# Optimization experiments

Measured on AMD Instinct MI355X. Metric: run time of the kernel, lower is better.

The kernel has to match this reference:

```python
import jax, jax.numpy as jnp
import numpy as np


def _attn_chunk(q, k, v, scale):
    # q: [b,s,h,d], k/v: [b,c,h,d] (one ring chunk)
    scores = jnp.einsum('bqhd,bkhd->bhqk', q, k) * scale
    lse = jax.nn.logsumexp(scores, axis=-1)            # [b,h,q]
    p = jnp.exp(scores - lse[..., None])               # [b,h,q,k]
    out = jnp.einsum('bhqk,bkhd->bqhd', p, v)          # [b,q,h,d]
    lse = jnp.transpose(lse, (0, 2, 1))[..., None]     # [b,q,h,1] for broadcast
    return out, lse


def setup_inputs() -> dict:
    key = jax.random.key(0)
    kq, kk, kv = jax.random.split(key, 3)
    B, S, H, D = 1, 4096, 16, 128
    q = jax.random.normal(kq, (B, S, H, D), dtype=jnp.float32)
    k = jax.random.normal(kk, (B, S, H, D), dtype=jnp.float32)
    v = jax.random.normal(kv, (B, S, H, D), dtype=jnp.float32)
    return {'q': q, 'k': k, 'v': v, 'ring_size': 4}


def reference(q, k, v, ring_size):
    # Ring attention forward: iterate over ring_size KV chunks, merging
    # partial (out, lse) with the sigmoid/logsigmoid online-softmax update
    # from update_out_and_lse_pass_q.
    B, S, H, D = q.shape
    R = int(ring_size)
    C = S // R
    scale = 1.0 / jnp.sqrt(jnp.asarray(D, dtype=q.dtype))
    k_chunks = k.reshape(B, R, C, H, D)
    v_chunks = v.reshape(B, R, C, H, D)

    # first ring step initializes the accumulators
    out, lse = _attn_chunk(q, k_chunks[:, 0], v_chunks[:, 0], scale)
    out = out.astype(jnp.float32)
    for r in range(1, R):
        block_out, block_lse = _attn_chunk(q, k_chunks[:, r], v_chunks[:, r], scale)
        block_out = block_out.astype(jnp.float32)
        # update_out_and_lse_pass_q
        out = out - jax.nn.sigmoid(block_lse - lse) * (out - block_out)
        lse = lse - jax.nn.log_sigmoid(lse - block_lse)
    return out
```

## Files before the change

kernel.cpp:

```cpp
#include <hip/hip_runtime.h>


#define S_LEN 4096
#define NH    16
#define DH    128
#define QT    128
#define KT    32
#define KSTR  136
#define VTS   40
#define QSTR  136
#define PSTR  40

typedef short bf16x8 __attribute__((ext_vector_type(8)));
typedef float floatx16 __attribute__((ext_vector_type(16)));

__device__ __forceinline__ unsigned short f2bf(float f) {
  union { float f; unsigned u; } x; x.f = f;
  unsigned r = x.u + 0x7FFFu + ((x.u >> 16) & 1u);
  return (unsigned short)(r >> 16);
}

__device__ __forceinline__ void gll16(const unsigned short* g, unsigned short* l) {
  __builtin_amdgcn_global_load_lds(
      (const __attribute__((address_space(1))) void*)g,
      (__attribute__((address_space(3))) void*)l, 16, 0, 0);
}

__global__ __launch_bounds__(256) void conv_k(const float* __restrict__ Kg,
                                              unsigned short* __restrict__ Kb) {
  int idx = blockIdx.x * 256 + threadIdx.x;
  int d4 = idx & 31;
  int h  = (idx >> 5) & 15;
  int s  = idx >> 9;
  float4 a = ((const float4*)Kg)[idx];
  ushort4 o = make_ushort4(f2bf(a.x), f2bf(a.y), f2bf(a.z), f2bf(a.w));
  ((ushort4*)Kb)[(((size_t)h * S_LEN + s) << 5) + d4] = o;
}

__global__ __launch_bounds__(256) void conv_v(const float* __restrict__ Vg,
                                              unsigned short* __restrict__ Vt) {
  __shared__ unsigned short sT[DH * VTS];
  const int c = blockIdx.x;
  const int h = blockIdx.y;
  const int t = threadIdx.x;
  {
    const int key = t >> 3;
    const int d0  = (t & 7) * 16;
    const int g   = (key >> 2) & 3;
    const int pos = (key & 3) | ((((g & 1) << 1) | (g >> 1)) << 2) | (key & 16);
    const float* src = Vg + (((size_t)(c * KT + key) * NH + h) * DH + d0);
#pragma unroll
    for (int i = 0; i < 4; ++i) {
      float4 a = ((const float4*)src)[i];
      sT[(d0 + 4 * i + 0) * VTS + pos] = f2bf(a.x);
      sT[(d0 + 4 * i + 1) * VTS + pos] = f2bf(a.y);
      sT[(d0 + 4 * i + 2) * VTS + pos] = f2bf(a.z);
      sT[(d0 + 4 * i + 3) * VTS + pos] = f2bf(a.w);
    }
  }
  __syncthreads();
  {
    const int d = t >> 1, hf = t & 1;
    uint4 w0 = *(const uint4*)&sT[d * VTS + hf * 16];
    uint4 w1 = *(const uint4*)&sT[d * VTS + hf * 16 + 8];
    size_t ob = ((size_t)(h * DH + d)) * S_LEN + c * KT + hf * 16;
    *(uint4*)&Vt[ob]     = w0;
    *(uint4*)&Vt[ob + 8] = w1;
  }
}

__global__ __launch_bounds__(256, 2) void fa_fwd3(
    const float* __restrict__ Qg, const unsigned short* __restrict__ Kb,
    const unsigned short* __restrict__ Vt, float* __restrict__ Og) {
  __shared__ __align__(16) unsigned short sK[2][4096];
  __shared__ __align__(16) unsigned short sV[2][4096];

  const int tid  = threadIdx.x;
  const int lane = tid & 63;
  const int wave = tid >> 6;
  const int f  = blockIdx.x;
  const int i  = f >> 3;
  const int h  = (f & 7) + 8 * (i & 1);
  const int q0 = (i >> 1) * QT;

  const unsigned short* Kh = Kb + (size_t)h * S_LEN * DH;
  const unsigned short* Vh = Vt + (size_t)h * DH * S_LEN;

  int skoff[2], svoff[2];
#pragma unroll
  for (int s = 0; s < 2; ++s) {
    const int ii = wave * 2 + s;
    { const int C = ii * 64 + lane;
      const int m = C >> 4;
      const int j = (lane & 15) ^ (m & 15);
      skoff[s] = m * DH + j * 8; }
    { const int C = ii * 64 + lane;
      const int r = C >> 2;
      const int j = (lane & 3) ^ ((r >> 1) & 3);
      svoff[s] = r * S_LEN + j * 8; }
  }
  const int ldst = wave * 1024;

  const int m31 = lane & 31, hh = lane >> 5;
  int kro[8], vro[8];
#pragma unroll
  for (int kc = 0; kc < 8; ++kc)
    kro[kc] = m31 * 128 + (((2 * kc + hh) ^ (m31 & 15)) * 8);
#pragma unroll
  for (int dt = 0; dt < 4; ++dt)
#pragma unroll
    for (int ff = 0; ff < 2; ++ff) {
      const int r = dt * 32 + m31;
      vro[dt * 2 + ff] = r * 32 + (((2 * ff + hh) ^ ((r >> 1) & 3)) * 8);
    }

  bf16x8 qf[8];
  {
    const float* qr = Qg +
        ((size_t)(q0 + wave * 32 + m31) * NH + h) * DH + hh * 8;
#pragma unroll
    for (int kc = 0; kc < 8; ++kc) {
      float4 a = *(const float4*)(qr + kc * 16);
      float4 b = *(const float4*)(qr + kc * 16 + 4);
      bf16x8 q;
      q[0] = f2bf(a.x); q[1] = f2bf(a.y); q[2] = f2bf(a.z); q[3] = f2bf(a.w);
      q[4] = f2bf(b.x); q[5] = f2bf(b.y); q[6] = f2bf(b.z); q[7] = f2bf(b.w);
      qf[kc] = q;
    }
  }

  floatx16 oacc[4];
#pragma unroll
  for (int dt = 0; dt < 4; ++dt)
#pragma unroll
    for (int j = 0; j < 16; ++j) oacc[dt][j] = 0.f;
  float ssum = 0.f;

#define ISSUE(BK, BV, KTV)                                                    \
  {                                                                           \
    _Pragma("unroll") for (int s = 0; s < 2; ++s) {                           \
      gll16(Kh + (size_t)(KTV) * DH + skoff[s], &(BK)[ldst + s * 512]);       \
      gll16(Vh + (KTV) + svoff[s], &(BV)[ldst + s * 512]);                    \
    }                                                                         \
  }

#define COMPUTE_TILE(KB, VB)                                                  \
  {                                                                           \
    floatx16 sc;                                                              \
    _Pragma("unroll") for (int j = 0; j < 16; ++j) sc[j] = 0.f;               \
    _Pragma("unroll") for (int kc = 0; kc < 8; ++kc) {                        \
      bf16x8 kf = *(const bf16x8*)((KB) + kro[kc]);                           \
      sc = __builtin_amdgcn_mfma_f32_32x32x16_bf16(kf, qf[kc], sc, 0, 0, 0);  \
    }                                                                         \
    float p[16];                                                              \
    _Pragma("unroll") for (int j = 0; j < 16; ++j) {                          \
      p[j] = __expf(fmaf(sc[j], 0.08838834764831845f, 0.0019512177f));        \
      ssum += p[j];                                                           \
    }                                                                         \
    bf16x8 pf0, pf1;                                                          \
    unsigned* u0 = (unsigned*)&pf0;                                           \
    unsigned* u1 = (unsigned*)&pf1;                                           \
    _Pragma("unroll") for (int m = 0; m < 4; ++m) {                           \
      u0[m] = (__float_as_uint(p[2 * m + 1]) & 0xFFFF0000u) |                 \
              (__float_as_uint(p[2 * m]) >> 16);                              \
      u1[m] = (__float_as_uint(p[2 * m + 9]) & 0xFFFF0000u) |                 \
              (__float_as_uint(p[2 * m + 8]) >> 16);                          \
    }                                                                         \
    _Pragma("unroll") for (int dt = 0; dt < 4; ++dt) {                        \
      bf16x8 v0 = *(const bf16x8*)((VB) + vro[dt * 2]);                       \
      bf16x8 v1 = *(const bf16x8*)((VB) + vro[dt * 2 + 1]);                   \
      oacc[dt] =                                                              \
          __builtin_amdgcn_mfma_f32_32x32x16_bf16(pf0, v0, oacc[dt], 0, 0, 0);\
      oacc[dt] =                                                              \
          __builtin_amdgcn_mfma_f32_32x32x16_bf16(pf1, v1, oacc[dt], 0, 0, 0);\
    }                                                                         \
  }

  ISSUE(sK[0], sV[0], 0);
  __syncthreads();
  for (int t = 0; t < 64; ++t) {
    ISSUE(sK[1], sV[1], 64 * t + 32);
    COMPUTE_TILE(sK[0], sV[0]);
    __syncthreads();
    if (t < 63) ISSUE(sK[0], sV[0], 64 * t + 64);
    COMPUTE_TILE(sK[1], sV[1]);
    __syncthreads();
  }
#undef ISSUE
#undef COMPUTE_TILE

  float tot  = ssum + __shfl_xor(ssum, 32);
  float vinv = 1.0f / tot;
  const int rb = hh * 4;
#pragma unroll
  for (int j = 0; j < 16; ++j) {
    const int row = (j & 3) + 8 * (j >> 2) + rb;
    const float inv = __shfl(vinv, row);
    float* op = Og + ((size_t)(q0 + wave * 32 + row) * NH + h) * DH + m31;
#pragma unroll
    for (int dt = 0; dt < 4; ++dt) op[dt * 32] = oacc[dt][j] * inv;
  }
}

__global__ __launch_bounds__(256, 2) void fa_fwd_v1(
    const float* __restrict__ Qg, const float* __restrict__ Kg,
    const float* __restrict__ Vg, float* __restrict__ Og)
{
  __shared__ unsigned short sQ[QT * QSTR];
  __shared__ unsigned short sK1[KT * KSTR];
  __shared__ unsigned short sVT1[DH * VTS];
  __shared__ unsigned short sP[4][32 * PSTR];
  const int tid  = threadIdx.x;
  const int lane = tid & 63;
  const int wave = tid >> 6;
  const int h    = blockIdx.y;
  const int q0   = blockIdx.x * QT;
  {
    const int row = tid >> 1;
    const int db  = (tid & 1) * 64;
    const float* gq = Qg + ((size_t)(q0 + row) * NH + h) * DH + db;
    unsigned short* dst = &sQ[row * QSTR + db];
#pragma unroll
    for (int i = 0; i < 16; ++i) {
      float4 a = ((const float4*)gq)[i];
      *(ushort4*)(dst + 4 * i) =
          make_ushort4(f2bf(a.x), f2bf(a.y), f2bf(a.z), f2bf(a.w));
    }
  }
  __syncthreads();
  bf16x8 qf[8];
  {
    const unsigned short* qr =
        &sQ[(wave * 32 + (lane & 31)) * QSTR + ((lane >> 5) * 8)];
#pragma unroll
    for (int kc = 0; kc < 8; ++kc) qf[kc] = *(const bf16x8*)(qr + kc * 16);
  }
  floatx16 oacc[4];
  float sl[16];
#pragma unroll
  for (int j = 0; j < 16; ++j) sl[j] = 0.f;
#pragma unroll
  for (int dt = 0; dt < 4; ++dt)
#pragma unroll
    for (int j = 0; j < 16; ++j) oacc[dt][j] = 0.f;
  for (int kt = 0; kt < S_LEN; kt += KT) {
    __syncthreads();
    {
      const int key = tid >> 3;
      const int db  = (tid & 7) * 16;
      const float* gk = Kg + ((size_t)(kt + key) * NH + h) * DH + db;
      unsigned short* dst = &sK1[key * KSTR + db];
#pragma unroll
      for (int i = 0; i < 4; ++i) {
        float4 a = ((const float4*)gk)[i];
        *(ushort4*)(dst + 4 * i) =
            make_ushort4(f2bf(a.x), f2bf(a.y), f2bf(a.z), f2bf(a.w));
      }
    }
    {
      const int kp = tid & 15;
      const int db = (tid >> 4) * 8;
      const float* g0 = Vg + ((size_t)(kt + 2 * kp) * NH + h) * DH + db;
      const float* g1 = g0 + (size_t)NH * DH;
      float4 a0 = ((const float4*)g0)[0], b0 = ((const float4*)g0)[1];
      float4 a1 = ((const float4*)g1)[0], b1 = ((const float4*)g1)[1];
      float e0[8] = {a0.x, a0.y, a0.z, a0.w, b0.x, b0.y, b0.z, b0.w};
      float e1[8] = {a1.x, a1.y, a1.z, a1.w, b1.x, b1.y, b1.z, b1.w};
      unsigned* dw = (unsigned*)sVT1;
#pragma unroll
      for (int j = 0; j < 8; ++j)
        dw[(db + j) * (VTS / 2) + kp] =
            (unsigned)f2bf(e0[j]) | ((unsigned)f2bf(e1[j]) << 16);
    }
    __syncthreads();
    floatx16 sc;
#pragma unroll
    for (int j = 0; j < 16; ++j) sc[j] = 0.f;
    {
      const unsigned short* kb = &sK1[(lane & 31) * KSTR + ((lane >> 5) * 8)];
#pragma unroll
      for (int kc = 0; kc < 8; ++kc) {
        bf16x8 bf = *(const bf16x8*)(kb + kc * 16);
        sc = __builtin_amdgcn_mfma_f32_32x32x16_bf16(qf[kc], bf, sc, 0, 0, 0);
      }
    }
    unsigned short pw[16];
#pragma unroll
    for (int j = 0; j < 16; ++j) {
      float p = __expf(sc[j] * 0.08838834764831845f);
      sl[j] += p;
      pw[j] = f2bf(p);
    }
    {
      unsigned short* pb = sP[wave];
      const int col = lane & 31;
      const int rb  = (lane >> 5) * 4;
#pragma unroll
      for (int j = 0; j < 16; ++j) {
        const int row = (j & 3) + 8 * (j >> 2) + rb;
        pb[row * PSTR + col] = pw[j];
      }
    }
    __syncthreads();
    bf16x8 pf0, pf1;
    {
      const unsigned short* pr =
          &sP[wave][(lane & 31) * PSTR + ((lane >> 5) * 8)];
      pf0 = *(const bf16x8*)(pr);
      pf1 = *(const bf16x8*)(pr + 16);
    }
#pragma unroll
    for (int dt = 0; dt < 4; ++dt) {
      const unsigned short* vb =
          &sVT1[(dt * 32 + (lane & 31)) * VTS + ((lane >> 5) * 8)];
      bf16x8 v0 = *(const bf16x8*)(vb);
      bf16x8 v1 = *(const bf16x8*)(vb + 16);
      oacc[dt] = __builtin_amdgcn_mfma_f32_32x32x16_bf16(pf0, v0, oacc[dt], 0, 0, 0);
      oacc[dt] = __builtin_amdgcn_mfma_f32_32x32x16_bf16(pf1, v1, oacc[dt], 0, 0, 0);
    }
  }
#pragma unroll
  for (int j = 0; j < 16; ++j) {
    float s = sl[j];
    s += __shfl_xor(s, 1);
    s += __shfl_xor(s, 2);
    s += __shfl_xor(s, 4);
    s += __shfl_xor(s, 8);
    s += __shfl_xor(s, 16);
    sl[j] = 1.0f / s;
  }
  {
    const int col = lane & 31;
    const int rb  = (lane >> 5) * 4;
#pragma unroll
    for (int j = 0; j < 16; ++j) {
      const int row = (j & 3) + 8 * (j >> 2) + rb;
      float* op = Og + ((size_t)(q0 + wave * 32 + row) * NH + h) * DH + col;
#pragma unroll
      for (int dt = 0; dt < 4; ++dt)
        op[dt * 32] = oacc[dt][j] * sl[j];
    }
  }
}

extern "C" void kernel_launch(void* const* d_in, const int* in_sizes, int n_in,
                              void* d_out, int out_size, void* d_ws, size_t ws_size,
                              hipStream_t stream) {
  const float* q = (const float*)d_in[0];
  const float* k = (const float*)d_in[1];
  const float* v = (const float*)d_in[2];
  float* o = (float*)d_out;
  const size_t elems = (size_t)NH * S_LEN * DH;
  const size_t need  = 2 * elems * sizeof(unsigned short);
  if (ws_size >= need) {
    unsigned short* Kb = (unsigned short*)d_ws;
    unsigned short* Vt = Kb + elems;
    conv_k<<<(int)(elems / 4 / 256), 256, 0, stream>>>(k, Kb);
    conv_v<<<dim3(S_LEN / KT, NH), 256, 0, stream>>>(v, Vt);
    fa_fwd3<<<512, 256, 0, stream>>>(q, Kb, Vt, o);
  } else {
    fa_fwd_v1<<<dim3(S_LEN / QT, NH), 256, 0, stream>>>(q, k, v, o);
  }
}
```

Baseline: 277.2 us.

## Split waves across key halves, reuse K/V fragments for two query tiles, merge in LDS

The main kernel now has each wave handle 64 query rows (two 32-row MFMA tiles) over half of each 64-key tile. Every K and V fragment read from LDS feeds two MFMAs, and LDS stages double to 64 KB with a shared-memory reduction of partial outputs and row sums at the end. The V transpose kernel drops its LDS staging and writes packed bf16 pairs straight to global memory. The bf16 packing uses a byte-permute instruction. The larger LDS footprint and doubled accumulators raise register and LDS pressure, which may limit occupancy, and the final merge adds extra synchronisation.

```diff
diff --git a/kernel.cpp b/kernel.cpp
--- a/kernel.cpp
+++ b/kernel.cpp
@@ -5,7 +5,6 @@
 #define NH    16
 #define DH    128
 #define QT    128
-#define KT    32
 #define KSTR  136
 #define VTS   40
 #define QSTR  136
@@ -18,6 +17,9 @@
   union { float f; unsigned u; } x; x.f = f;
   unsigned r = x.u + 0x7FFFu + ((x.u >> 16) & 1u);
   return (unsigned short)(r >> 16);
+}
+__device__ __forceinline__ unsigned packbf(float a, float b) {
+  return (unsigned)f2bf(a) | ((unsigned)f2bf(b) << 16);
 }
 
 __device__ __forceinline__ void gll16(const unsigned short* g, unsigned short* l) {
@@ -38,46 +40,39 @@
 }
 
 __global__ __launch_bounds__(256) void conv_v(const float* __restrict__ Vg,
-                                              unsigned short* __restrict__ Vt) {
-  __shared__ unsigned short sT[DH * VTS];
-  const int c = blockIdx.x;
-  const int h = blockIdx.y;
-  const int t = threadIdx.x;
-  {
-    const int key = t >> 3;
-    const int d0  = (t & 7) * 16;
-    const int g   = (key >> 2) & 3;
-    const int pos = (key & 3) | ((((g & 1) << 1) | (g >> 1)) << 2) | (key & 16);
-    const float* src = Vg + (((size_t)(c * KT + key) * NH + h) * DH + d0);
-#pragma unroll
-    for (int i = 0; i < 4; ++i) {
-      float4 a = ((const float4*)src)[i];
-      sT[(d0 + 4 * i + 0) * VTS + pos] = f2bf(a.x);
-      sT[(d0 + 4 * i + 1) * VTS + pos] = f2bf(a.y);
-      sT[(d0 + 4 * i + 2) * VTS + pos] = f2bf(a.z);
-      sT[(d0 + 4 * i + 3) * VTS + pos] = f2bf(a.w);
-    }
-  }
-  __syncthreads();
-  {
-    const int d = t >> 1, hf = t & 1;
-    uint4 w0 = *(const uint4*)&sT[d * VTS + hf * 16];
-    uint4 w1 = *(const uint4*)&sT[d * VTS + hf * 16 + 8];
-    size_t ob = ((size_t)(h * DH + d)) * S_LEN + c * KT + hf * 16;
-    *(uint4*)&Vt[ob]     = w0;
-    *(uint4*)&Vt[ob + 8] = w1;
-  }
-}
-
-__global__ __launch_bounds__(256, 2) void fa_fwd3(
+                                              unsigned* __restrict__ Vtd) {
+  const int c  = blockIdx.x;
+  const int hd = blockIdx.y;
+  const int t  = threadIdx.x;
+  const int kp   = t & 15;
+  const int d0   = (t >> 4) * 8;
+  const int key0 = 2 * kp;
+  const int g    = (key0 >> 2) & 3;
+  const int pos0 = (key0 & 3) | ((((g & 1) << 1) | (g >> 1)) << 2) | (key0 & 16);
+  const float* s0 = Vg + ((size_t)(c * 32 + key0) * NH + hd) * DH + d0;
+  const float* s1 = s0 + (size_t)NH * DH;
+  float4 a0 = ((const float4*)s0)[0], b0 = ((const float4*)s0)[1];
+  float4 a1 = ((const float4*)s1)[0], b1 = ((const float4*)s1)[1];
+  float e0[8] = {a0.x, a0.y, a0.z, a0.w, b0.x, b0.y, b0.z, b0.w};
+  float e1[8] = {a1.x, a1.y, a1.z, a1.w, b1.x, b1.y, b1.z, b1.w};
+  unsigned* dst = Vtd + ((size_t)(hd * DH + d0)) * (S_LEN / 2) + c * 16 + (pos0 >> 1);
+#pragma unroll
+  for (int j = 0; j < 8; ++j)
+    dst[j * (S_LEN / 2)] = packbf(e0[j], e1[j]);
+}
+
+__global__ __launch_bounds__(256, 2) void fa_fwd4(
     const float* __restrict__ Qg, const unsigned short* __restrict__ Kb,
     const unsigned short* __restrict__ Vt, float* __restrict__ Og) {
-  __shared__ __align__(16) unsigned short sK[2][4096];
-  __shared__ __align__(16) unsigned short sV[2][4096];
+  __shared__ __align__(16) unsigned char smem[65536];
+  unsigned short* sKb = (unsigned short*)smem;
+  unsigned short* sVb = (unsigned short*)(smem + 32768);
 
   const int tid  = threadIdx.x;
   const int lane = tid & 63;
   const int wave = tid >> 6;
+  const int qg   = wave >> 1;
+  const int kh   = wave & 1;
   const int f  = blockIdx.x;
   const int i  = f >> 3;
   const int h  = (f & 7) + 8 * (i & 1);
@@ -89,13 +84,11 @@
   int skoff[2], svoff[2];
 #pragma unroll
   for (int s = 0; s < 2; ++s) {
-    const int ii = wave * 2 + s;
-    { const int C = ii * 64 + lane;
-      const int m = C >> 4;
+    const int C = (wave * 2 + s) * 64 + lane;
+    { const int m = C >> 4;
       const int j = (lane & 15) ^ (m & 15);
       skoff[s] = m * DH + j * 8; }
-    { const int C = ii * 64 + lane;
-      const int r = C >> 2;
+    { const int r = C >> 2;
       const int j = (lane & 3) ^ ((r >> 1) & 3);
       svoff[s] = r * S_LEN + j * 8; }
   }
@@ -113,11 +106,14 @@
       const int r = dt * 32 + m31;
       vro[dt * 2 + ff] = r * 32 + (((2 * ff + hh) ^ ((r >> 1) & 3)) * 8);
     }
-
-  bf16x8 qf[8];
-  {
+  const unsigned short* kBase[2] = {sKb + kh * 4096, sKb + 8192 + kh * 4096};
+  const unsigned short* vBase[2] = {sVb + kh * 4096, sVb + 8192 + kh * 4096};
+
+  bf16x8 qf[2][8];
+#pragma unroll
+  for (int s = 0; s < 2; ++s) {
     const float* qr = Qg +
-        ((size_t)(q0 + wave * 32 + m31) * NH + h) * DH + hh * 8;
+        ((size_t)(q0 + qg * 64 + s * 32 + m31) * NH + h) * DH + hh * 8;
 #pragma unroll
     for (int kc = 0; kc < 8; ++kc) {
       float4 a = *(const float4*)(qr + kc * 16);
@@ -125,80 +121,128 @@
       bf16x8 q;
       q[0] = f2bf(a.x); q[1] = f2bf(a.y); q[2] = f2bf(a.z); q[3] = f2bf(a.w);
       q[4] = f2bf(b.x); q[5] = f2bf(b.y); q[6] = f2bf(b.z); q[7] = f2bf(b.w);
-      qf[kc] = q;
-    }
-  }
-
-  floatx16 oacc[4];
-#pragma unroll
-  for (int dt = 0; dt < 4; ++dt)
-#pragma unroll
-    for (int j = 0; j < 16; ++j) oacc[dt][j] = 0.f;
-  float ssum = 0.f;
-
-#define ISSUE(BK, BV, KTV)                                                    \
+      qf[s][kc] = q;
+    }
+  }
+
+  floatx16 oa[2][4];
+#pragma unroll
+  for (int s = 0; s < 2; ++s)
+#pragma unroll
+    for (int dt = 0; dt < 4; ++dt)
+#pragma unroll
+      for (int j = 0; j < 16; ++j) oa[s][dt][j] = 0.f;
+  float ss0 = 0.f, ss1 = 0.f;
+
+#define ISSUE64(BUF, KT0)                                                     \
   {                                                                           \
-    _Pragma("unroll") for (int s = 0; s < 2; ++s) {                           \
-      gll16(Kh + (size_t)(KTV) * DH + skoff[s], &(BK)[ldst + s * 512]);       \
-      gll16(Vh + (KTV) + svoff[s], &(BV)[ldst + s * 512]);                    \
+    _Pragma("unroll") for (int hlf = 0; hlf < 2; ++hlf)                       \
+    _Pragma("unroll") for (int s2 = 0; s2 < 2; ++s2) {                        \
+      gll16(Kh + (size_t)((KT0) + hlf * 32) * DH + skoff[s2],                 \
+            sKb + (BUF) * 8192 + hlf * 4096 + ldst + s2 * 512);               \
+      gll16(Vh + ((KT0) + hlf * 32) + svoff[s2],                              \
+            sVb + (BUF) * 8192 + hlf * 4096 + ldst + s2 * 512);               \
     }                                                                         \
   }
 
-#define COMPUTE_TILE(KB, VB)                                                  \
+#define COMPUTE64(B)                                                          \
   {                                                                           \
-    floatx16 sc;                                                              \
-    _Pragma("unroll") for (int j = 0; j < 16; ++j) sc[j] = 0.f;               \
+    const unsigned short* KB = kBase[B];                                      \
+    const unsigned short* VB = vBase[B];                                      \
+    floatx16 sc0, sc1;                                                        \
+    _Pragma("unroll") for (int j = 0; j < 16; ++j) { sc0[j] = 0.f; sc1[j] = 0.f; } \
     _Pragma("unroll") for (int kc = 0; kc < 8; ++kc) {                        \
-      bf16x8 kf = *(const bf16x8*)((KB) + kro[kc]);                           \
-      sc = __builtin_amdgcn_mfma_f32_32x32x16_bf16(kf, qf[kc], sc, 0, 0, 0);  \
+      bf16x8 kf = *(const bf16x8*)(KB + kro[kc]);                             \
+      sc0 = __builtin_amdgcn_mfma_f32_32x32x16_bf16(kf, qf[0][kc], sc0, 0, 0, 0); \
+      sc1 = __builtin_amdgcn_mfma_f32_32x32x16_bf16(kf, qf[1][kc], sc1, 0, 0, 0); \
     }                                                                         \
-    float p[16];                                                              \
+    float p0[16], p1[16];                                                     \
     _Pragma("unroll") for (int j = 0; j < 16; ++j) {                          \
-      p[j] = __expf(fmaf(sc[j], 0.08838834764831845f, 0.0019512177f));        \
-      ssum += p[j];                                                           \
+      p0[j] = __expf(fmaf(sc0[j], 0.08838834764831845f, 0.0019512177f));      \
+      ss0 += p0[j];                                                           \
+      p1[j] = __expf(fmaf(sc1[j], 0.08838834764831845f, 0.0019512177f));      \
+      ss1 += p1[j];                                                           \
     }                                                                         \
-    bf16x8 pf0, pf1;                                                          \
-    unsigned* u0 = (unsigned*)&pf0;                                           \
-    unsigned* u1 = (unsigned*)&pf1;                                           \
+    bf16x8 pfA0, pfA1, pfB0, pfB1;                                            \
+    unsigned* uA0 = (unsigned*)&pfA0; unsigned* uA1 = (unsigned*)&pfA1;       \
+    unsigned* uB0 = (unsigned*)&pfB0; unsigned* uB1 = (unsigned*)&pfB1;       \
     _Pragma("unroll") for (int m = 0; m < 4; ++m) {                           \
-      u0[m] = (__float_as_uint(p[2 * m + 1]) & 0xFFFF0000u) |                 \
-              (__float_as_uint(p[2 * m]) >> 16);                              \
-      u1[m] = (__float_as_uint(p[2 * m + 9]) & 0xFFFF0000u) |                 \
-              (__float_as_uint(p[2 * m + 8]) >> 16);                          \
+      uA0[m] = __builtin_amdgcn_perm(__float_as_uint(p0[2 * m + 1]),          \
+                                     __float_as_uint(p0[2 * m]), 0x07060302u);\
+      uA1[m] = __builtin_amdgcn_perm(__float_as_uint(p0[2 * m + 9]),          \
+                                     __float_as_uint(p0[2 * m + 8]), 0x07060302u);\
+      uB0[m] = __builtin_amdgcn_perm(__float_as_uint(p1[2 * m + 1]),          \
+                                     __float_as_uint(p1[2 * m]), 0x07060302u);\
+      uB1[m] = __builtin_amdgcn_perm(__float_as_uint(p1[2 * m + 9]),          \
+                                     __float_as_uint(p1[2 * m + 8]), 0x07060302u);\
     }                                                                         \
     _Pragma("unroll") for (int dt = 0; dt < 4; ++dt) {                        \
-      bf16x8 v0 = *(const bf16x8*)((VB) + vro[dt * 2]);                       \
-      bf16x8 v1 = *(const bf16x8*)((VB) + vro[dt * 2 + 1]);                   \
-      oacc[dt] =                                                              \
-          __builtin_amdgcn_mfma_f32_32x32x16_bf16(pf0, v0, oacc[dt], 0, 0, 0);\
-      oacc[dt] =                                                              \
-          __builtin_amdgcn_mfma_f32_32x32x16_bf16(pf1, v1, oacc[dt], 0, 0, 0);\
+      bf16x8 v0 = *(const bf16x8*)(VB + vro[dt * 2]);                         \
+      bf16x8 v1 = *(const bf16x8*)(VB + vro[dt * 2 + 1]);                     \
+      oa[0][dt] = __builtin_amdgcn_mfma_f32_32x32x16_bf16(pfA0, v0, oa[0][dt], 0, 0, 0); \
+      oa[0][dt] = __builtin_amdgcn_mfma_f32_32x32x16_bf16(pfA1, v1, oa[0][dt], 0, 0, 0); \
+      oa[1][dt] = __builtin_amdgcn_mfma_f32_32x32x16_bf16(pfB0, v0, oa[1][dt], 0, 0, 0); \
+      oa[1][dt] = __builtin_amdgcn_mfma_f32_32x32x16_bf16(pfB1, v1, oa[1][dt], 0, 0, 0); \
     }                                                                         \
   }
 
-  ISSUE(sK[0], sV[0], 0);
+  ISSUE64(0, 0);
   __syncthreads();
-  for (int t = 0; t < 64; ++t) {
-    ISSUE(sK[1], sV[1], 64 * t + 32);
-    COMPUTE_TILE(sK[0], sV[0]);
-    __syncthreads();
-    if (t < 63) ISSUE(sK[0], sV[0], 64 * t + 64);
-    COMPUTE_TILE(sK[1], sV[1]);
-    __syncthreads();
-  }
-#undef ISSUE
-#undef COMPUTE_TILE
-
-  float tot  = ssum + __shfl_xor(ssum, 32);
-  float vinv = 1.0f / tot;
-  const int rb = hh * 4;
-#pragma unroll
-  for (int j = 0; j < 16; ++j) {
-    const int row = (j & 3) + 8 * (j >> 2) + rb;
-    const float inv = __shfl(vinv, row);
-    float* op = Og + ((size_t)(q0 + wave * 32 + row) * NH + h) * DH + m31;
-#pragma unroll
-    for (int dt = 0; dt < 4; ++dt) op[dt * 32] = oacc[dt][j] * inv;
+  for (int t = 0; t < 32; ++t) {
+    ISSUE64(1, t * 128 + 64);
+    COMPUTE64(0);
+    __syncthreads();
+    if (t < 31) ISSUE64(0, t * 128 + 128);
+    COMPUTE64(1);
+    __syncthreads();
+  }
+#undef ISSUE64
+#undef COMPUTE64
+
+  float tt0 = ss0 + __shfl_xor(ss0, 32);
+  float tt1 = ss1 + __shfl_xor(ss1, 32);
+  float* mrg = (float*)smem;
+  float* sSm = (float*)(smem + 40960);
+#pragma unroll
+  for (int s = 0; s < 2; ++s) {
+    const float tts = s ? tt1 : tt0;
+    __syncthreads();
+    if (kh == 1) {
+      float* w = mrg + qg * 4352 + lane * 68;
+#pragma unroll
+      for (int dt = 0; dt < 4; ++dt)
+#pragma unroll
+        for (int j4 = 0; j4 < 4; ++j4) {
+          float4 vv = make_float4(oa[s][dt][j4 * 4 + 0], oa[s][dt][j4 * 4 + 1],
+                                  oa[s][dt][j4 * 4 + 2], oa[s][dt][j4 * 4 + 3]);
+          *(float4*)(w + dt * 16 + j4 * 4) = vv;
+        }
+      if (hh == 0) sSm[qg * 32 + m31] = tts;
+    }
+    __syncthreads();
+    if (kh == 0) {
+      const float* r = mrg + qg * 4352 + lane * 68;
+#pragma unroll
+      for (int dt = 0; dt < 4; ++dt)
+#pragma unroll
+        for (int j4 = 0; j4 < 4; ++j4) {
+          float4 vv = *(const float4*)(r + dt * 16 + j4 * 4);
+          oa[s][dt][j4 * 4 + 0] += vv.x;
+          oa[s][dt][j4 * 4 + 1] += vv.y;
+          oa[s][dt][j4 * 4 + 2] += vv.z;
+          oa[s][dt][j4 * 4 + 3] += vv.w;
+        }
+      float vinv = 1.0f / (tts + sSm[qg * 32 + m31]);
+#pragma unroll
+      for (int j = 0; j < 16; ++j) {
+        const int row = (j & 3) + 8 * (j >> 2) + hh * 4;
+        const float inv = __shfl(vinv, row);
+        float* op = Og +
+            ((size_t)(q0 + qg * 64 + s * 32 + row) * NH + h) * DH + m31;
+#pragma unroll
+        for (int dt = 0; dt < 4; ++dt) op[dt * 32] = oa[s][dt][j] * inv;
+      }
+    }
   }
 }
 
@@ -207,7 +251,7 @@
     const float* __restrict__ Vg, float* __restrict__ Og)
 {
   __shared__ unsigned short sQ[QT * QSTR];
-  __shared__ unsigned short sK1[KT * KSTR];
+  __shared__ unsigned short sK1[32 * KSTR];
   __shared__ unsigned short sVT1[DH * VTS];
   __shared__ unsigned short sP[4][32 * PSTR];
   const int tid  = threadIdx.x;
@@ -243,7 +287,7 @@
   for (int dt = 0; dt < 4; ++dt)
 #pragma unroll
     for (int j = 0; j < 16; ++j) oacc[dt][j] = 0.f;
-  for (int kt = 0; kt < S_LEN; kt += KT) {
+  for (int kt = 0; kt < S_LEN; kt += 32) {
     __syncthreads();
     {
       const int key = tid >> 3;
@@ -269,8 +313,7 @@
       unsigned* dw = (unsigned*)sVT1;
 #pragma unroll
       for (int j = 0; j < 8; ++j)
-        dw[(db + j) * (VTS / 2) + kp] =
-            (unsigned)f2bf(e0[j]) | ((unsigned)f2bf(e1[j]) << 16);
+        dw[(db + j) * (VTS / 2) + kp] = packbf(e0[j], e1[j]);
     }
     __syncthreads();
     floatx16 sc;
@@ -356,8 +399,8 @@
     unsigned short* Kb = (unsigned short*)d_ws;
     unsigned short* Vt = Kb + elems;
     conv_k<<<(int)(elems / 4 / 256), 256, 0, stream>>>(k, Kb);
-    conv_v<<<dim3(S_LEN / KT, NH), 256, 0, stream>>>(v, Vt);
-    fa_fwd3<<<512, 256, 0, stream>>>(q, Kb, Vt, o);
+    conv_v<<<dim3(S_LEN / 32, NH), 256, 0, stream>>>(v, (unsigned*)Vt);
+    fa_fwd4<<<512, 256, 0, stream>>>(q, Kb, Vt, o);
   } else {
     fa_fwd_v1<<<dim3(S_LEN / QT, NH), 256, 0, stream>>>(q, k, v, o);
   }
```

Result: slower. 353.8 us (+27.6%).
